# Optimization experiments

Hardware: AMD Instinct MI355X
Metric: run time of the kernel (lower is better)

The kernel has to match this reference:

```python
import jax, jax.numpy as jnp
import numpy as np

H, DK, DV = 16, 64, 64  # head_nums, key_size, head_size
D_MODEL = H * DK        # 1024
OUT_DIM = H * DV        # 1024


def setup_inputs() -> dict:
    key = jax.random.key(0)
    ks = jax.random.split(key, 12)
    B, S = 2, 2048
    scale = 0.02
    return {
        "q": jax.random.normal(ks[0], (B, S, D_MODEL), jnp.float32),
        "k": jax.random.normal(ks[1], (B, S, D_MODEL), jnp.float32),
        "v": jax.random.normal(ks[2], (B, S, D_MODEL), jnp.float32),
        "Wq": jax.random.normal(ks[3], (D_MODEL, H * DK), jnp.float32) * scale,
        "bq": jnp.zeros((H * DK,), jnp.float32),
        "Wk": jax.random.normal(ks[4], (D_MODEL, H * DK), jnp.float32) * scale,
        "bk": jnp.zeros((H * DK,), jnp.float32),
        "Wv": jax.random.normal(ks[5], (D_MODEL, OUT_DIM), jnp.float32) * scale,
        "bv": jnp.zeros((OUT_DIM,), jnp.float32),
        "Wo": jax.random.normal(ks[6], (OUT_DIM, OUT_DIM), jnp.float32) * scale,
        "bo": jnp.zeros((OUT_DIM,), jnp.float32),
    }


def reference(q, k, v, Wq, bq, Wk, bk, Wv, bv, Wo, bo):
    B, S, _ = q.shape
    # linear projections, split heads
    qw = (q @ Wq + bq).reshape(B, S, H, DK)   # [B,S,H,dk]
    kw = (k @ Wk + bk).reshape(B, S, H, DK)   # [B,S,H,dk]
    vw = (v @ Wv + bv).reshape(B, S, H, DV)   # [B,S,H,dv]
    # scaled dot-product attention scores
    att = jnp.einsum("bshk,bqhk->bhsq", qw, kw) / (DK ** 0.5)  # [B,H,S,S]
    att = jax.nn.softmax(att, axis=-1)
    out = jnp.einsum("bhsq,bqhk->bhsk", att, vw)  # [B,H,S,dv]
    out = out.transpose(0, 2, 1, 3).reshape(B, S, OUT_DIM)  # merge heads
    return out @ Wo + bo
```

## Files before the change

### kernel.cpp

```cpp
#include <hip/hip_runtime.h>
#include <hip/hip_bf16.h>

#define BB 2
#define SS 2048
#define HH 16
#define DD 64
#define DM 1024
#define MM (BB*SS)

typedef __attribute__((ext_vector_type(4))) float f32x4;
typedef __attribute__((ext_vector_type(16))) float f32x16;
typedef __attribute__((ext_vector_type(8))) short s16x8;
typedef __attribute__((ext_vector_type(2))) int i32x2;

__device__ __forceinline__ unsigned short f2bf(float f){
  unsigned int u = __float_as_uint(f);
  u += 0x7FFF + ((u >> 16) & 1);
  return (unsigned short)(u >> 16);
}

__device__ __forceinline__ f32x4 zero4(){ f32x4 z = {0.f,0.f,0.f,0.f}; return z; }

__device__ __forceinline__ unsigned int cvtpk(float a, float b){
  unsigned int r;
  asm("v_cvt_pk_bf16_f32 %0, %1, %2" : "=v"(r) : "v"(a), "v"(b));
  return r;
}

__device__ __forceinline__ void gload_lds16(const void* g, void* l){
  __builtin_amdgcn_global_load_lds(
    (const __attribute__((address_space(1))) unsigned int*)g,
    (__attribute__((address_space(3))) unsigned int*)l, 16, 0, 0);
}

__global__ __launch_bounds__(256) void wtrans_kernel(
    const float* __restrict__ Wq, const float* __restrict__ Wk,
    const float* __restrict__ Wv, const float* __restrict__ Wo,
    short* __restrict__ wt){
  __shared__ float tile[64][65];
  const float* src = (blockIdx.y==0)?Wq:(blockIdx.y==1)?Wk:(blockIdx.y==2)?Wv:Wo;
  short* dst = wt + (size_t)blockIdx.y * ((size_t)DM*DM);
  int tk = (blockIdx.x >> 4) * 64;
  int tn = (blockIdx.x & 15) * 64;
  int t = threadIdx.x;
  int r = t >> 2;
  int c4 = (t & 3) << 4;
  const float* p = src + (size_t)(tk + r) * DM + tn + c4;
  #pragma unroll
  for (int i = 0; i < 4; ++i){
    float4 vv = *(const float4*)(p + i*4);
    tile[r][c4 + i*4 + 0] = vv.x;
    tile[r][c4 + i*4 + 1] = vv.y;
    tile[r][c4 + i*4 + 2] = vv.z;
    tile[r][c4 + i*4 + 3] = vv.w;
  }
  __syncthreads();
  s16x8 o0, o1;
  #pragma unroll
  for (int j = 0; j < 8; ++j) o0[j] = (short)f2bf(tile[c4 + j][r]);
  #pragma unroll
  for (int j = 0; j < 8; ++j) o1[j] = (short)f2bf(tile[c4 + 8 + j][r]);
  short* qd = dst + (size_t)(tn + r) * DM + tk + c4;
  *(s16x8*)qd       = o0;
  *(s16x8*)(qd + 8) = o1;
}

#define GEMM_PRE_COMMON() \
  int m0 = blockIdx.x * 128, n0 = blockIdx.y * 64; \
  int t = threadIdx.x; \
  int w = t >> 6, lane = t & 63, g = lane >> 4, c = lane & 15; \
  int wm = (w >> 1) * 64, wn = (w & 1) * 32; \
  f32x4 acc[4][2]; \
  _Pragma("unroll") for (int i=0;i<4;++i) \
    _Pragma("unroll") for (int j=0;j<2;++j) acc[i][j] = zero4(); \
  int srow = t >> 3; \
  int scol = ((t & 7) ^ (srow & 7)) * 8; \
  const short* Bp = BT + (size_t)(n0 + srow) * DM + scol; \
  int rsw = (c & 7) << 4; \
  int adst = srow*128 + (t & 7)*16;

#define BSTAGE(k0_, BB_) { \
  gload_lds16(Bp + (k0_),          (char*)(BB_) + w*1024); \
  gload_lds16(Bp + 32*DM + (k0_),  (char*)(BB_) + 4096 + w*1024); \
}

#define ALOAD_F32(k0_) { \
  _Pragma("unroll") for (int ch=0; ch<4; ++ch){ \
    areg[2*ch]   = *(const float4*)(Apf + (size_t)ch*32*DM + (k0_)); \
    areg[2*ch+1] = *(const float4*)(Apf + (size_t)ch*32*DM + (k0_) + 4); \
  } }

#define AWRITE(AB_) { \
  _Pragma("unroll") for (int ch=0; ch<4; ++ch){ \
    int4 pk4; \
    pk4.x = (int)cvtpk(areg[2*ch].x,   areg[2*ch].y); \
    pk4.y = (int)cvtpk(areg[2*ch].z,   areg[2*ch].w); \
    pk4.z = (int)cvtpk(areg[2*ch+1].x, areg[2*ch+1].y); \
    pk4.w = (int)cvtpk(areg[2*ch+1].z, areg[2*ch+1].w); \
    *(int4*)((char*)(AB_) + ch*4096 + adst) = pk4; \
  } }

#define ASTAGE_BF16(k0_, AB_) { \
  gload_lds16(Apb + (k0_),          (char*)(AB_) + w*1024); \
  gload_lds16(Apb + 32*DM + (k0_),  (char*)(AB_) + 4096  + w*1024); \
  gload_lds16(Apb + 64*DM + (k0_),  (char*)(AB_) + 8192  + w*1024); \
  gload_lds16(Apb + 96*DM + (k0_),  (char*)(AB_) + 12288 + w*1024); \
}

#define GCOMP(AB_, BB_) { \
  s16x8 af[4][2], bfr[2][2]; \
  _Pragma("unroll") for (int mi=0;mi<4;++mi){ \
    const char* arow = (const char*)(AB_) + (wm + mi*16 + c)*128; \
    af[mi][0] = *(const s16x8*)(arow + ((g*16) ^ rsw)); \
    af[mi][1] = *(const s16x8*)(arow + ((64 + g*16) ^ rsw)); \
  } \
  _Pragma("unroll") for (int ni=0;ni<2;++ni){ \
    const char* brow = (const char*)(BB_) + (wn + ni*16 + c)*128; \
    bfr[ni][0] = *(const s16x8*)(brow + ((g*16) ^ rsw)); \
    bfr[ni][1] = *(const s16x8*)(brow + ((64 + g*16) ^ rsw)); \
  } \
  _Pragma("unroll") for (int mi=0;mi<4;++mi) \
    _Pragma("unroll") for (int ni=0;ni<2;++ni){ \
      acc[mi][ni] = __builtin_amdgcn_mfma_f32_16x16x32_bf16(af[mi][0], bfr[ni][0], acc[mi][ni], 0,0,0); \
      acc[mi][ni] = __builtin_amdgcn_mfma_f32_16x16x32_bf16(af[mi][1], bfr[ni][1], acc[mi][ni], 0,0,0); \
    } \
}

#define GEMM_LOOP_F32() \
  float4 areg[8]; \
  ALOAD_F32(0) \
  BSTAGE(0, &Bs[0][0]) \
  AWRITE(&As[0][0]) \
  __syncthreads(); \
  for (int kk = 0; kk < DM; kk += 128){ \
    if (kk + 64 < DM){ ALOAD_F32(kk+64) BSTAGE(kk+64, &Bs[1][0]) } \
    GCOMP(&As[0][0], &Bs[0][0]) \
    if (kk + 64 < DM){ AWRITE(&As[1][0]) } \
    __syncthreads(); \
    if (kk + 128 < DM){ ALOAD_F32(kk+128) BSTAGE(kk+128, &Bs[0][0]) } \
    GCOMP(&As[1][0], &Bs[1][0]) \
    if (kk + 128 < DM){ AWRITE(&As[0][0]) } \
    __syncthreads(); \
  }

#define GEMM_LOOP_BF16() \
  ASTAGE_BF16(0, &As[0][0]) \
  BSTAGE(0, &Bs[0][0]) \
  __syncthreads(); \
  for (int kk = 0; kk < DM; kk += 128){ \
    if (kk + 64 < DM){ ASTAGE_BF16(kk+64, &As[1][0]) BSTAGE(kk+64, &Bs[1][0]) } \
    GCOMP(&As[0][0], &Bs[0][0]) \
    __syncthreads(); \
    if (kk + 128 < DM){ ASTAGE_BF16(kk+128, &As[0][0]) BSTAGE(kk+128, &Bs[0][0]) } \
    GCOMP(&As[1][0], &Bs[1][0]) \
    __syncthreads(); \
  }

__global__ __launch_bounds__(256) void gemm_qkv3_kernel(
    const float* __restrict__ qs, const float* __restrict__ ks,
    const float* __restrict__ vs, const short* __restrict__ WT3,
    const float* __restrict__ bq, const float* __restrict__ bk,
    const float* __restrict__ bv,
    short* __restrict__ Qh, short* __restrict__ Kh, short* __restrict__ Vt,
    float qscale){
  __shared__ __align__(16) short As[2][128*64];
  __shared__ __align__(16) short Bs[2][64*64];
  int z = blockIdx.z;
  const float* A    = (z==0) ? qs : (z==1) ? ks : vs;
  const short* BT   = WT3 + (size_t)z * ((size_t)DM*DM);
  const float* bias = (z==0) ? bq : (z==1) ? bk : bv;
  GEMM_PRE_COMMON()
  const float* Apf = A + (size_t)(m0 + srow) * DM + scol;
  GEMM_LOOP_F32()
  if (z < 2){
    short* outh = (z==0) ? Qh : Kh;
    float scale = (z==0) ? qscale : 1.0f;
    #pragma unroll
    for (int ni=0;ni<2;++ni){
      int col = n0 + wn + ni*16 + c;
      float bvv = bias[col];
      int hh = col >> 6, d = col & 63;
      #pragma unroll
      for (int mi=0;mi<4;++mi){
        #pragma unroll
        for (int r=0;r<4;++r){
          int row = m0 + wm + mi*16 + g*4 + r;
          int b = row >> 11, s = row & (SS-1);
          float val = (acc[mi][ni][r] + bvv) * scale;
          outh[((((size_t)b*HH + hh)*SS + s) << 6) + d] = (short)f2bf(val);
        }
      }
    }
  } else {
    #pragma unroll
    for (int ni=0;ni<2;++ni){
      int col = n0 + wn + ni*16 + c;
      float bvv = bias[col];
      int hh = col >> 6, d = col & 63;
      #pragma unroll
      for (int mi=0;mi<4;++mi){
        int row = m0 + wm + mi*16 + g*4;
        int b = row >> 11, s = row & (SS-1);
        i32x2 pk2;
        pk2.x = (int)cvtpk(acc[mi][ni][0] + bvv, acc[mi][ni][1] + bvv);
        pk2.y = (int)cvtpk(acc[mi][ni][2] + bvv, acc[mi][ni][3] + bvv);
        *(i32x2*)(Vt + (((size_t)(b*HH + hh)*64 + d) * SS + s)) = pk2;
      }
    }
  }
}

__global__ __launch_bounds__(256) void gemm_out_kernel(
    const short* __restrict__ A, const short* __restrict__ BT,
    const float* __restrict__ bias, float* __restrict__ out){
  __shared__ __align__(16) short As[2][128*64];
  __shared__ __align__(16) short Bs[2][64*64];
  GEMM_PRE_COMMON()
  const short* Apb = A + (size_t)(m0 + srow) * DM + scol;
  GEMM_LOOP_BF16()
  #pragma unroll
  for (int ni=0;ni<2;++ni){
    int col = n0 + wn + ni*16 + c;
    float bvv = bias[col];
    #pragma unroll
    for (int mi=0;mi<4;++mi){
      #pragma unroll
      for (int r=0;r<4;++r){
        int row = m0 + wm + mi*16 + g*4 + r;
        out[(size_t)row * DM + col] = acc[mi][ni][r] + bvv;
      }
    }
  }
}

__global__ __launch_bounds__(256) void attn_kernel(
    const short* __restrict__ Qh, const short* __restrict__ Kh,
    const short* __restrict__ Vt, short* __restrict__ Oh){
  __shared__ __align__(16) short SMEM[16384];
  int bh = blockIdx.y;
  int qb = blockIdx.x * 128;
  int t = threadIdx.x, w = t >> 6, lane = t & 63;
  int lq = lane & 31, h = lane >> 5;
  int qrow0 = qb + w*32;

  const short* qg = Qh + (((size_t)bh*SS + qrow0 + lq) << 6) + h*8;
  s16x8 qf[4];
  #pragma unroll
  for (int kc=0;kc<4;++kc) qf[kc] = *(const s16x8*)(qg + kc*16);

  f32x16 z16;
  #pragma unroll
  for (int i=0;i<16;++i) z16[i] = 0.f;
  f32x16 oA, oB;
  #pragma unroll
  for (int i=0;i<16;++i){ oA[i]=0.f; oB[i]=0.f; }
  float l = 0.f;
  const char* kbase = (const char*)(Kh + (((size_t)bh*SS) << 6));
  const char* vbase = (const char*)(Vt + ((size_t)bh*64) * SS);

  int rsel = lane >> 3;
  int csw  = ((lane & 7) << 4) ^ (rsel << 4);
  int swr  = (lane & 7) << 4;

  const char* smem = (const char*)&SMEM[0];
  const char* kr0 = smem + lq*128 + (( 0 + h*16) ^ swr);
  const char* kr1 = smem + lq*128 + ((32 + h*16) ^ swr);
  const char* kr2 = smem + lq*128 + ((64 + h*16) ^ swr);
  const char* kr3 = smem + lq*128 + ((96 + h*16) ^ swr);
  char* smem_w = (char*)&SMEM[0] + w*2048;

#define STAGE(T, BOFF) { \
    const char* kg = kbase + (((size_t)((T)*64 + w*16 + rsel)) << 7) + csw; \
    gload_lds16(kg,        smem_w + (BOFF)); \
    gload_lds16(kg + 1024, smem_w + (BOFF) + 1024); \
    const char* vg = vbase + (size_t)(w*16 + rsel) * (SS*2) + ((size_t)(T) << 7) + csw; \
    gload_lds16(vg,            smem_w + (BOFF) + 16384); \
    gload_lds16(vg + 8*(SS*2), smem_w + (BOFF) + 16384 + 1024); \
  }

#define MFMA32(a_, b_, c_) __builtin_amdgcn_mfma_f32_32x32x16_bf16(a_, b_, c_, 0,0,0)

#define TILE(BOFF) { \
    f32x16 sA, sB; \
    s16x8 kf; \
    __builtin_amdgcn_s_setprio(1); \
    kf = *(const s16x8*)(kr0 + (BOFF));        sA = MFMA32(kf, qf[0], z16); \
    kf = *(const s16x8*)(kr0 + (BOFF) + 4096); sB = MFMA32(kf, qf[0], z16); \
    kf = *(const s16x8*)(kr1 + (BOFF));        sA = MFMA32(kf, qf[1], sA); \
    kf = *(const s16x8*)(kr1 + (BOFF) + 4096); sB = MFMA32(kf, qf[1], sB); \
    kf = *(const s16x8*)(kr2 + (BOFF));        sA = MFMA32(kf, qf[2], sA); \
    kf = *(const s16x8*)(kr2 + (BOFF) + 4096); sB = MFMA32(kf, qf[2], sB); \
    kf = *(const s16x8*)(kr3 + (BOFF));        sA = MFMA32(kf, qf[3], sA); \
    kf = *(const s16x8*)(kr3 + (BOFF) + 4096); sB = MFMA32(kf, qf[3], sB); \
    __builtin_amdgcn_s_setprio(0); \
    float lp = 0.f; \
    unsigned int cA[8], cB[8]; \
    _Pragma("unroll") \
    for (int i=0;i<8;++i){ \
      float a0 = __builtin_amdgcn_exp2f(sA[2*i]); \
      float a1 = __builtin_amdgcn_exp2f(sA[2*i+1]); \
      float b0 = __builtin_amdgcn_exp2f(sB[2*i]); \
      float b1 = __builtin_amdgcn_exp2f(sB[2*i+1]); \
      lp += (a0 + a1) + (b0 + b1); \
      cA[i] = cvtpk(a0, a1); \
      cB[i] = cvtpk(b0, b1); \
    } \
    l += lp; \
    asm("v_permlane32_swap_b32 %0, %1" : "+v"(cA[0]), "+v"(cA[2])); \
    asm("v_permlane32_swap_b32 %0, %1" : "+v"(cA[1]), "+v"(cA[3])); \
    asm("v_permlane32_swap_b32 %0, %1" : "+v"(cA[4]), "+v"(cA[6])); \
    asm("v_permlane32_swap_b32 %0, %1" : "+v"(cA[5]), "+v"(cA[7])); \
    asm("v_permlane32_swap_b32 %0, %1" : "+v"(cB[0]), "+v"(cB[2])); \
    asm("v_permlane32_swap_b32 %0, %1" : "+v"(cB[1]), "+v"(cB[3])); \
    asm("v_permlane32_swap_b32 %0, %1" : "+v"(cB[4]), "+v"(cB[6])); \
    asm("v_permlane32_swap_b32 %0, %1" : "+v"(cB[5]), "+v"(cB[7])); \
    s16x8 pbf0, pbf1, pbf2, pbf3; \
    { unsigned int* p0 = (unsigned int*)&pbf0; \
      p0[0]=cA[0]; p0[1]=cA[1]; p0[2]=cA[2]; p0[3]=cA[3]; \
      unsigned int* p1 = (unsigned int*)&pbf1; \
      p1[0]=cA[4]; p1[1]=cA[5]; p1[2]=cA[6]; p1[3]=cA[7]; \
      unsigned int* p2 = (unsigned int*)&pbf2; \
      p2[0]=cB[0]; p2[1]=cB[1]; p2[2]=cB[2]; p2[3]=cB[3]; \
      unsigned int* p3 = (unsigned int*)&pbf3; \
      p3[0]=cB[4]; p3[1]=cB[5]; p3[2]=cB[6]; p3[3]=cB[7]; } \
    __builtin_amdgcn_s_setprio(1); \
    kf = *(const s16x8*)(kr0 + (BOFF) + 16384);        oA = MFMA32(kf, pbf0, oA); \
    kf = *(const s16x8*)(kr0 + (BOFF) + 16384 + 4096); oB = MFMA32(kf, pbf0, oB); \
    kf = *(const s16x8*)(kr1 + (BOFF) + 16384);        oA = MFMA32(kf, pbf1, oA); \
    kf = *(const s16x8*)(kr1 + (BOFF) + 16384 + 4096); oB = MFMA32(kf, pbf1, oB); \
    kf = *(const s16x8*)(kr2 + (BOFF) + 16384);        oA = MFMA32(kf, pbf2, oA); \
    kf = *(const s16x8*)(kr2 + (BOFF) + 16384 + 4096); oB = MFMA32(kf, pbf2, oB); \
    kf = *(const s16x8*)(kr3 + (BOFF) + 16384);        oA = MFMA32(kf, pbf3, oA); \
    kf = *(const s16x8*)(kr3 + (BOFF) + 16384 + 4096); oB = MFMA32(kf, pbf3, oB); \
    __builtin_amdgcn_s_setprio(0); \
  }

  STAGE(0, 0)
  __syncthreads();

  for (int tb = 0; tb < 32; tb += 2){
    STAGE(tb+1, 8192)
    TILE(0)
    __syncthreads();
    if (tb + 2 < 32) STAGE(tb+2, 0)
    TILE(8192)
    __syncthreads();
  }
#undef STAGE
#undef TILE

  l += __shfl_xor(l, 32);
  float inv = 1.f / l;
  int b = bh >> 4, hh = bh & 15;
  short* ob = Oh + (((size_t)(b*SS + qrow0 + lq)) << 10) + hh*64 + 4*h;
  #pragma unroll
  for (int rg=0;rg<4;++rg){
    i32x2 pk;
    pk.x = (int)cvtpk(oA[rg*4+0]*inv, oA[rg*4+1]*inv);
    pk.y = (int)cvtpk(oA[rg*4+2]*inv, oA[rg*4+3]*inv);
    *(i32x2*)(ob + 8*rg) = pk;
    pk.x = (int)cvtpk(oB[rg*4+0]*inv, oB[rg*4+1]*inv);
    pk.y = (int)cvtpk(oB[rg*4+2]*inv, oB[rg*4+3]*inv);
    *(i32x2*)(ob + 32 + 8*rg) = pk;
  }
}

extern "C" void kernel_launch(void* const* d_in, const int* in_sizes, int n_in,
                              void* d_out, int out_size, void* d_ws, size_t ws_size,
                              hipStream_t stream){
  const float* q  = (const float*)d_in[0];
  const float* k  = (const float*)d_in[1];
  const float* v  = (const float*)d_in[2];
  const float* Wq = (const float*)d_in[3];
  const float* bq = (const float*)d_in[4];
  const float* Wk = (const float*)d_in[5];
  const float* bk = (const float*)d_in[6];
  const float* Wv = (const float*)d_in[7];
  const float* bv = (const float*)d_in[8];
  const float* Wo = (const float*)d_in[9];
  const float* bo = (const float*)d_in[10];
  (void)in_sizes; (void)n_in; (void)out_size; (void)ws_size;

  short* wsp = (short*)d_ws;
  const size_t MW = 1048576;
  short* WT3 = wsp;
  short* WTo = wsp + 3*MW;
  short* Qh  = wsp + 4*MW;
  short* Kh  = wsp + 8*MW;
  short* Oh  = wsp + 12*MW;
  short* Vt  = wsp + 16*MW;

  const float QSCALE = 0.125f * 1.44269504088896f;
  wtrans_kernel<<<dim3(256,4), 256, 0, stream>>>(Wq, Wk, Wv, Wo, wsp);
  gemm_qkv3_kernel<<<dim3(32,16,3), 256, 0, stream>>>(q, k, v, WT3, bq, bk, bv,
                                                      Qh, Kh, Vt, QSCALE);
  attn_kernel<<<dim3(16,32), 256, 0, stream>>>(Qh, Kh, Vt, Oh);
  gemm_out_kernel<<<dim3(32,16), 256, 0, stream>>>(Oh, WTo, bo, (float*)d_out);
}
```

Before: 123.2 us.

## Split attention KV range across wave pairs and reduce partial outputs in LDS

```diff
diff --git a/kernel.cpp b/kernel.cpp
--- a/kernel.cpp
+++ b/kernel.cpp
@@ -236,12 +236,13 @@
 __global__ __launch_bounds__(256) void attn_kernel(
     const short* __restrict__ Qh, const short* __restrict__ Kh,
     const short* __restrict__ Vt, short* __restrict__ Oh){
-  __shared__ __align__(16) short SMEM[16384];
+  __shared__ __align__(16) short SMEM[32768];
   int bh = blockIdx.y;
-  int qb = blockIdx.x * 128;
+  int qb = blockIdx.x * 64;
   int t = threadIdx.x, w = t >> 6, lane = t & 63;
   int lq = lane & 31, h = lane >> 5;
-  int qrow0 = qb + w*32;
+  int wq = w >> 1, wz = w & 1;
+  int qrow0 = qb + wq*32;
 
   const short* qg = Qh + (((size_t)bh*SS + qrow0 + lq) << 6) + h*8;
   s16x8 qf[4];
@@ -263,20 +264,24 @@
   int swr  = (lane & 7) << 4;
 
   const char* smem = (const char*)&SMEM[0];
-  const char* kr0 = smem + lq*128 + (( 0 + h*16) ^ swr);
-  const char* kr1 = smem + lq*128 + ((32 + h*16) ^ swr);
-  const char* kr2 = smem + lq*128 + ((64 + h*16) ^ swr);
-  const char* kr3 = smem + lq*128 + ((96 + h*16) ^ swr);
-  char* smem_w = (char*)&SMEM[0] + w*2048;
+  const char* kr0 = smem + wz*8192 + lq*128 + (( 0 + h*16) ^ swr);
+  const char* kr1 = smem + wz*8192 + lq*128 + ((32 + h*16) ^ swr);
+  const char* kr2 = smem + wz*8192 + lq*128 + ((64 + h*16) ^ swr);
+  const char* kr3 = smem + wz*8192 + lq*128 + ((96 + h*16) ^ swr);
+  char* sdst = (char*)&SMEM[0] + wz*8192 + wq*16384;
 
 #define STAGE(T, BOFF) { \
-    const char* kg = kbase + (((size_t)((T)*64 + w*16 + rsel)) << 7) + csw; \
-    gload_lds16(kg,        smem_w + (BOFF)); \
-    gload_lds16(kg + 1024, smem_w + (BOFF) + 1024); \
-    const char* vg = vbase + (size_t)(w*16 + rsel) * (SS*2) + ((size_t)(T) << 7) + csw; \
-    gload_lds16(vg,            smem_w + (BOFF) + 16384); \
-    gload_lds16(vg + 8*(SS*2), smem_w + (BOFF) + 16384 + 1024); \
-  }
+    if (wq == 0){ \
+      _Pragma("unroll") for (int i=0;i<8;++i){ \
+        const char* kg = kbase + (((size_t)((T)*64 + i*8 + rsel)) << 7) + csw; \
+        gload_lds16(kg, sdst + (BOFF) + i*1024); \
+      } \
+    } else { \
+      _Pragma("unroll") for (int i=0;i<8;++i){ \
+        const char* vg = vbase + (size_t)(i*8 + rsel) * (SS*2) + (((size_t)(T)) << 7) + csw; \
+        gload_lds16(vg, sdst + (BOFF) + i*1024); \
+      } \
+    } }
 
 #define MFMA32(a_, b_, c_) __builtin_amdgcn_mfma_f32_32x32x16_bf16(a_, b_, c_, 0,0,0)
 
@@ -335,33 +340,52 @@
     __builtin_amdgcn_s_setprio(0); \
   }
 
-  STAGE(0, 0)
+  int T0 = wz * 16;
+  STAGE(T0, 0)
   __syncthreads();
 
-  for (int tb = 0; tb < 32; tb += 2){
-    STAGE(tb+1, 8192)
+  for (int tb = 0; tb < 16; tb += 2){
+    STAGE(T0 + tb + 1, 32768)
     TILE(0)
     __syncthreads();
-    if (tb + 2 < 32) STAGE(tb+2, 0)
-    TILE(8192)
+    if (tb + 2 < 16) STAGE(T0 + tb + 2, 0)
+    TILE(32768)
     __syncthreads();
   }
 #undef STAGE
 #undef TILE
 
   l += __shfl_xor(l, 32);
-  float inv = 1.f / l;
-  int b = bh >> 4, hh = bh & 15;
-  short* ob = Oh + (((size_t)(b*SS + qrow0 + lq)) << 10) + hh*64 + 4*h;
-  #pragma unroll
-  for (int rg=0;rg<4;++rg){
-    i32x2 pk;
-    pk.x = (int)cvtpk(oA[rg*4+0]*inv, oA[rg*4+1]*inv);
-    pk.y = (int)cvtpk(oA[rg*4+2]*inv, oA[rg*4+3]*inv);
-    *(i32x2*)(ob + 8*rg) = pk;
-    pk.x = (int)cvtpk(oB[rg*4+0]*inv, oB[rg*4+1]*inv);
-    pk.y = (int)cvtpk(oB[rg*4+2]*inv, oB[rg*4+3]*inv);
-    *(i32x2*)(ob + 32 + 8*rg) = pk;
+
+  float* shf = (float*)&SMEM[0];
+  float* slot = shf + ((size_t)wq*64 + lane) * 33;
+  if (wz == 1){
+    #pragma unroll
+    for (int i=0;i<16;++i) slot[i]      = oA[i];
+    #pragma unroll
+    for (int i=0;i<16;++i) slot[16 + i] = oB[i];
+    slot[32] = l;
+  }
+  __syncthreads();
+  if (wz == 0){
+    #pragma unroll
+    for (int i=0;i<16;++i) oA[i] += slot[i];
+    #pragma unroll
+    for (int i=0;i<16;++i) oB[i] += slot[16 + i];
+    l += slot[32];
+    float inv = 1.f / l;
+    int b = bh >> 4, hh = bh & 15;
+    short* ob = Oh + (((size_t)(b*SS + qrow0 + lq)) << 10) + hh*64 + 4*h;
+    #pragma unroll
+    for (int rg=0;rg<4;++rg){
+      i32x2 pk;
+      pk.x = (int)cvtpk(oA[rg*4+0]*inv, oA[rg*4+1]*inv);
+      pk.y = (int)cvtpk(oA[rg*4+2]*inv, oA[rg*4+3]*inv);
+      *(i32x2*)(ob + 8*rg) = pk;
+      pk.x = (int)cvtpk(oB[rg*4+0]*inv, oB[rg*4+1]*inv);
+      pk.y = (int)cvtpk(oB[rg*4+2]*inv, oB[rg*4+3]*inv);
+      *(i32x2*)(ob + 32 + 8*rg) = pk;
+    }
   }
 }
 
@@ -394,6 +418,6 @@
   wtrans_kernel<<<dim3(256,4), 256, 0, stream>>>(Wq, Wk, Wv, Wo, wsp);
   gemm_qkv3_kernel<<<dim3(32,16,3), 256, 0, stream>>>(q, k, v, WT3, bq, bk, bv,
                                                       Qh, Kh, Vt, QSCALE);
-  attn_kernel<<<dim3(16,32), 256, 0, stream>>>(Qh, Kh, Vt, Oh);
+  attn_kernel<<<dim3(32,32), 256, 0, stream>>>(Qh, Kh, Vt, Oh);
   gemm_out_kernel<<<dim3(32,16), 256, 0, stream>>>(Oh, WTo, bo, (float*)d_out);
 }
```

After: 129.2 us. +4.8%, slower.
